# Kernel optimization log

Hardware: AMD Instinct MI355X
Metric: run time of the kernel (lower is better)

## Reference

```python
import jax, jax.numpy as jnp
import numpy as np

B, N, D, H, DH = 1, 192, 128, 4, 32
INNER = H * DH  # == D


def _ln(x, g, b):
    mu = x.mean(-1, keepdims=True)
    var = ((x - mu) ** 2).mean(-1, keepdims=True)
    return (x - mu) * jax.lax.rsqrt(var + 1e-5) * g + b


def _axial(x, row, lng, lnb, wq, wkv, wo, bo, wg, bg, wb):
    # x: (B, N, N, D). row=True: attend along axis 2 (rows as batch);
    # row=False: attend along axis 1 (columns as batch).
    scale = DH ** -0.5
    # edge bias from RAW x (edges are not layer-normed in the torch code)
    bias = jnp.einsum('bijd,dh->bhij', x, wb)            # (B, H, N, N)
    xn = _ln(x, lng, lnb)
    xa = xn if row else jnp.swapaxes(xn, 1, 2)           # (B, R, S, D)
    q = (xa @ wq).reshape(B, N, N, H, DH) * scale
    kv = (xa @ wkv).reshape(B, N, N, 2, H, DH)           # chunk(2): k then v
    k, v = kv[..., 0, :, :], kv[..., 1, :, :]
    # scores: (B, R, H, q, k); same bias matrix broadcast over every row/col R
    dots = jnp.einsum('brqhe,brkhe->brhqk', q, k) + bias[:, None]
    attn = jax.nn.softmax(dots, axis=-1)
    o = jnp.einsum('brhqk,brkhe->brqhe', attn, v).reshape(B, N, N, INNER)
    gates = jax.nn.sigmoid(xa @ wg + bg)                 # sigmoid gating on pre-attn x
    out = (o * gates) @ wo + bo
    return out if row else jnp.swapaxes(out, 1, 2)


def setup_inputs() -> dict:
    key = jax.random.key(0)
    ks = iter(jax.random.split(key, 32))

    def w(shape, s=0.02):
        return jax.random.normal(next(ks), shape, dtype=jnp.float32) * s

    inp = {"x": jax.random.normal(next(ks), (B, N, N, D), dtype=jnp.float32)}
    for sfx in ("o", "i"):  # outgoing (row) / ingoing (col) triangle attention
        inp[f"lng_{sfx}"] = jnp.ones((D,), jnp.float32)
        inp[f"lnb_{sfx}"] = jnp.zeros((D,), jnp.float32)
        inp[f"wq_{sfx}"] = w((D, INNER))
        inp[f"wkv_{sfx}"] = w((D, 2 * INNER))
        inp[f"wo_{sfx}"] = w((INNER, D))
        inp[f"bo_{sfx}"] = jnp.zeros((D,), jnp.float32)
        inp[f"wg_{sfx}"] = w((D, INNER))
        inp[f"bg_{sfx}"] = jnp.ones((INNER,), jnp.float32)  # gating bias init = 1
        inp[f"wb_{sfx}"] = w((D, H))
    inp["lng_f"] = jnp.ones((D,), jnp.float32)
    inp["lnb_f"] = jnp.zeros((D,), jnp.float32)
    inp["w1"] = w((D, 8 * D))      # dim -> dim*mult*2, mult=4
    inp["b1"] = jnp.zeros((8 * D,), jnp.float32)
    inp["w2"] = w((4 * D, D))
    inp["b2"] = jnp.zeros((D,), jnp.float32)
    return inp


def reference(x, lng_o, lnb_o, wq_o, wkv_o, wo_o, bo_o, wg_o, bg_o, wb_o,
              lng_i, lnb_i, wq_i, wkv_i, wo_i, bo_i, wg_i, bg_i, wb_i,
              lng_f, lnb_f, w1, b1, w2, b2):
    x = _axial(x, True, lng_o, lnb_o, wq_o, wkv_o, wo_o, bo_o, wg_o, bg_o, wb_o) + x
    x = _axial(x, False, lng_i, lnb_i, wq_i, wkv_i, wo_i, bo_i, wg_i, bg_i, wb_i) + x
    xn = _ln(x, lng_f, lnb_f)
    h = xn @ w1 + b1
    a, g = jnp.split(h, 2, axis=-1)   # GEGLU: x * gelu(gates), exact gelu
    ff = (a * jax.nn.gelu(g, approximate=False)) @ w2 + b2
    return x + ff
```

## Files before the change

kernel.cpp:

```cpp
#include <hip/hip_runtime.h>
#include <hip/hip_bf16.h>
#include <math.h>

constexpr int NSEQ = 192;
constexpr int DIM  = 128;
constexpr int NH   = 4;
constexpr int DHEAD = 32;
constexpr int MROWS = NSEQ * NSEQ;

typedef __hip_bfloat16 bf16;
typedef __attribute__((ext_vector_type(8))) short bf16x8;
typedef __attribute__((ext_vector_type(4))) float f32x4;
typedef unsigned int u32;

__device__ __forceinline__ void gload16(const void* g, void* l) {
    __builtin_amdgcn_global_load_lds(
        (const __attribute__((address_space(1))) u32*)g,
        (__attribute__((address_space(3))) u32*)l, 16, 0, 0);
}

__device__ __forceinline__ short f2bs(float f) {
    __hip_bfloat16 h = __float2bfloat16(f);
    return *(short*)&h;
}

__global__ __launch_bounds__(256)
void convert_weights(const float* __restrict__ wq_o, const float* __restrict__ wkv_o,
                     const float* __restrict__ wg_o,
                     const float* __restrict__ wq_i, const float* __restrict__ wkv_i,
                     const float* __restrict__ wg_i,
                     const float* __restrict__ wo_o, const float* __restrict__ wo_i,
                     const float* __restrict__ w1, const float* __restrict__ b1,
                     const float* __restrict__ w2,
                     bf16* __restrict__ WQKVG_O, bf16* __restrict__ WQKVG_I,
                     bf16* __restrict__ WOT_O, bf16* __restrict__ WOT_I,
                     bf16* __restrict__ W1PT, bf16* __restrict__ W2T,
                     float* __restrict__ B1P)
{
    int idx = blockIdx.x * 256 + threadIdx.x;
    const float scale = 0.17677669529663689f;
    if (idx < 131072) {
        int s = idx >> 16, i = idx & 65535;
        int r = i >> 7, d = i & 127;
        const float* wq  = s ? wq_i  : wq_o;
        const float* wkv = s ? wkv_i : wkv_o;
        const float* wg  = s ? wg_i  : wg_o;
        float v;
        if (r < 128)      v = wq[d * 128 + r] * scale;
        else if (r < 384) v = wkv[d * 256 + (r - 128)];
        else              v = wg[d * 128 + (r - 384)];
        (s ? WQKVG_I : WQKVG_O)[i] = __float2bfloat16(v);
    } else if (idx < 163840) {
        int i = idx - 131072; int s = i >> 14; i &= 16383;
        int r = i >> 7, d = i & 127;
        (s ? WOT_I : WOT_O)[i] = __float2bfloat16((s ? wo_i : wo_o)[d * 128 + r]);
    } else if (idx < 294912) {
        int i = idx - 163840;
        int r = i >> 7, d = i & 127;
        int col = (r & 1) ? 512 + (r >> 1) : (r >> 1);
        W1PT[i] = __float2bfloat16(w1[d * 1024 + col]);
    } else if (idx < 360448) {
        int i = idx - 294912;
        int n = i >> 9, k = i & 511;
        W2T[i] = __float2bfloat16(w2[k * 128 + n]);
    } else if (idx < 361472) {
        int r = idx - 360448;
        B1P[r] = b1[(r & 1) ? 512 + (r >> 1) : (r >> 1)];
    }
}

__global__ __launch_bounds__(256)
void ln_bias_kernel(const float* __restrict__ x, const float* __restrict__ g,
                    const float* __restrict__ b, const float* __restrict__ wb,
                    bf16* __restrict__ xa, float* __restrict__ bias)
{
    int wid  = threadIdx.x >> 6;
    int lane = threadIdx.x & 63;
    int row  = blockIdx.x * 4 + wid;
    const float* xr = x + (size_t)row * DIM;
    float x0 = xr[lane], x1 = xr[lane + 64];
    float s = x0 + x1, sq = x0 * x0 + x1 * x1;
    #pragma unroll
    for (int off = 32; off > 0; off >>= 1) {
        s  += __shfl_down(s, off);
        sq += __shfl_down(sq, off);
    }
    s = __shfl(s, 0); sq = __shfl(sq, 0);
    float mu  = s * (1.0f / 128.0f);
    float var = sq * (1.0f / 128.0f) - mu * mu;
    float rs  = rsqrtf(var + 1e-5f);
    float y0 = (x0 - mu) * rs * g[lane]      + b[lane];
    float y1 = (x1 - mu) * rs * g[lane + 64] + b[lane + 64];
    bf16* yr = xa + (size_t)row * DIM;
    yr[lane]      = __float2bfloat16(y0);
    yr[lane + 64] = __float2bfloat16(y1);
    #pragma unroll
    for (int h = 0; h < NH; ++h) {
        float bh = x0 * wb[lane * NH + h] + x1 * wb[(lane + 64) * NH + h];
        #pragma unroll
        for (int off = 32; off > 0; off >>= 1) bh += __shfl_down(bh, off);
        if (lane == 0) bias[(size_t)h * MROWS + row] = bh;
    }
}

enum { EPI_QKVG = 0, EPI_OUT = 1, EPI_GEGLU = 2, EPI_FF2 = 3 };

template<int EPI, int BM, int K>
__global__ __launch_bounds__(256, 4)
void mfma_gemm(const bf16* __restrict__ A, const bf16* __restrict__ BT,
               const float* __restrict__ e_bias,
               const float* __restrict__ e_resid,
               float* __restrict__ e_outf,
               bf16* __restrict__ e_outb,
               bf16* __restrict__ e_outb2,
               const float* __restrict__ lng,
               const float* __restrict__ lnb,
               const float* __restrict__ wbp,
               float* __restrict__ biasb,
               bf16* __restrict__ xa,
               int trans)
{
    constexpr int MREP  = BM / 32;
    constexpr int AB    = BM * 128;
    constexpr int STAGE = AB + 16384;
    constexpr int EPIB  = (BM / 2) * 512;
    constexpr int LDSB  = STAGE > EPIB ? STAGE : EPIB;
    __shared__ char sm[LDSB];
    char* asb = sm;
    char* bsb = sm + AB;
    float* eb = (float*)sm;

    int tid = threadIdx.x;
    int l = tid & 63, w = tid >> 6;
    int wr = w >> 1, wc = w & 1;
    int m0 = blockIdx.x * BM, n0 = blockIdx.y * 128;
    int fr = l & 15, g = l >> 4;
    int lr8 = l >> 3;
    int satom = (l & 7) ^ lr8;

    f32x4 acc[MREP][4] = {};

    for (int k0 = 0; k0 < K; k0 += 64) {
        #pragma unroll
        for (int i = 0; i < BM / 32; ++i)
            gload16(A + (size_t)(m0 + i * 32 + w * 8 + lr8) * K + k0 + satom * 8,
                    asb + i * 4096 + w * 1024);
        #pragma unroll
        for (int i = 0; i < 4; ++i)
            gload16(BT + (size_t)(n0 + i * 32 + w * 8 + lr8) * K + k0 + satom * 8,
                    bsb + i * 4096 + w * 1024);
        __syncthreads();
        #pragma unroll
        for (int kk = 0; kk < 2; ++kk) {
            bf16x8 af[MREP], bfr[4];
            #pragma unroll
            for (int mi = 0; mi < MREP; ++mi) {
                int r = wr * (BM / 2) + mi * 16 + fr;
                af[mi] = *(const bf16x8*)(asb + r * 128 + ((kk * 64 + g * 16) ^ ((r & 7) << 4)));
            }
            #pragma unroll
            for (int ni = 0; ni < 4; ++ni) {
                int r = wc * 64 + ni * 16 + fr;
                bfr[ni] = *(const bf16x8*)(bsb + r * 128 + ((kk * 64 + g * 16) ^ ((r & 7) << 4)));
            }
            #pragma unroll
            for (int mi = 0; mi < MREP; ++mi)
                #pragma unroll
                for (int ni = 0; ni < 4; ++ni)
                    acc[mi][ni] = __builtin_amdgcn_mfma_f32_16x16x32_bf16(
                        af[mi], bfr[ni], acc[mi][ni], 0, 0, 0);
        }
        __syncthreads();
    }

    #pragma unroll
    for (int rr = 0; rr < 2; ++rr) {
        if (wr == rr) {
            #pragma unroll
            for (int mi = 0; mi < MREP; ++mi)
                #pragma unroll
                for (int ni = 0; ni < 4; ++ni)
                    #pragma unroll
                    for (int j = 0; j < 4; ++j) {
                        int rl = mi * 16 + g * 4 + j;
                        int cl = wc * 64 + ni * 16 + fr;
                        int a  = cl >> 2;
                        int pa = (((a >> 2) + (a & 3)) & 7) | ((a & 3) << 3);
                        eb[rl * 128 + pa * 4 + (cl & 3)] = acc[mi][ni][j];
                    }
        }
        __syncthreads();
        #pragma unroll
        for (int p = 0; p < BM / 64; ++p) {
            int c = tid + p * 256;
            int row_l = c >> 3, ch = c & 7;
            int grow = m0 + rr * (BM / 2) + row_l;
            int gc0 = ch * 16;
            float v[16];
            #pragma unroll
            for (int q = 0; q < 4; ++q) {
                int pa = ((ch + q) & 7) + q * 8;
                f32x4 t4 = *(const f32x4*)&eb[row_l * 128 + pa * 4];
                v[q * 4 + 0] = t4[0]; v[q * 4 + 1] = t4[1];
                v[q * 4 + 2] = t4[2]; v[q * 4 + 3] = t4[3];
            }
            if (EPI == EPI_QKVG) {
                int seg = blockIdx.y;
                short o16[16];
                if (seg < 3) {
                    #pragma unroll
                    for (int i = 0; i < 16; ++i) o16[i] = f2bs(v[i]);
                    int h = ch >> 1, e0 = (ch & 1) * 16;
                    bf16* dst = e_outb + ((size_t)(seg * NH + h) * MROWS + grow) * DHEAD + e0;
                    *(uint4*)dst = *(uint4*)o16;
                    *(uint4*)(dst + 8) = *(uint4*)(o16 + 8);
                } else {
                    #pragma unroll
                    for (int i = 0; i < 16; ++i)
                        o16[i] = f2bs(1.0f / (1.0f + __expf(-(v[i] + e_bias[gc0 + i]))));
                    bf16* dst = e_outb2 + (size_t)grow * DIM + gc0;
                    *(uint4*)dst = *(uint4*)o16;
                    *(uint4*)(dst + 8) = *(uint4*)(o16 + 8);
                }
            } else if (EPI == EPI_OUT) {
                int orow  = trans ? ((grow % NSEQ) * NSEQ + grow / NSEQ) : grow;
                int xarow = (grow % NSEQ) * NSEQ + grow / NSEQ;
                const float* rp = e_resid + (size_t)orow * DIM + gc0;
                float* op = e_outf + (size_t)orow * DIM + gc0;
                #pragma unroll
                for (int q = 0; q < 4; ++q) {
                    float4 r4 = *(const float4*)(rp + q * 4);
                    v[q*4+0] += e_bias[gc0 + q*4 + 0] + r4.x;
                    v[q*4+1] += e_bias[gc0 + q*4 + 1] + r4.y;
                    v[q*4+2] += e_bias[gc0 + q*4 + 2] + r4.z;
                    v[q*4+3] += e_bias[gc0 + q*4 + 3] + r4.w;
                    *(float4*)(op + q * 4) = make_float4(v[q*4+0], v[q*4+1], v[q*4+2], v[q*4+3]);
                }
                float s1 = 0.f, s2 = 0.f;
                #pragma unroll
                for (int i = 0; i < 16; ++i) { s1 += v[i]; s2 += v[i] * v[i]; }
                #pragma unroll
                for (int off = 1; off < 8; off <<= 1) {
                    s1 += __shfl_xor(s1, off);
                    s2 += __shfl_xor(s2, off);
                }
                float mu  = s1 * (1.0f / 128.0f);
                float var = s2 * (1.0f / 128.0f) - mu * mu;
                float rs  = rsqrtf(var + 1e-5f);
                short o16[16];
                #pragma unroll
                for (int i = 0; i < 16; ++i)
                    o16[i] = f2bs((v[i] - mu) * rs * lng[gc0 + i] + lnb[gc0 + i]);
                bf16* xd = xa + (size_t)xarow * DIM + gc0;
                *(uint4*)xd = *(uint4*)o16;
                *(uint4*)(xd + 8) = *(uint4*)(o16 + 8);
                if (wbp) {
                    float bh[NH] = {};
                    #pragma unroll
                    for (int i = 0; i < 16; ++i) {
                        float vv = v[i];
                        #pragma unroll
                        for (int h = 0; h < NH; ++h)
                            bh[h] = fmaf(vv, wbp[(gc0 + i) * NH + h], bh[h]);
                    }
                    #pragma unroll
                    for (int off = 1; off < 8; off <<= 1)
                        #pragma unroll
                        for (int h = 0; h < NH; ++h) bh[h] += __shfl_xor(bh[h], off);
                    if (ch == 0)
                        #pragma unroll
                        for (int h = 0; h < NH; ++h)
                            biasb[(size_t)h * MROWS + grow] = bh[h];
                }
            } else if (EPI == EPI_FF2) {
                const float* rp = e_resid + (size_t)grow * DIM + gc0;
                float* op = e_outf + (size_t)grow * DIM + gc0;
                #pragma unroll
                for (int q = 0; q < 4; ++q) {
                    float4 r4 = *(const float4*)(rp + q * 4);
                    float4 o4;
                    o4.x = v[q*4+0] + e_bias[gc0 + q*4 + 0] + r4.x;
                    o4.y = v[q*4+1] + e_bias[gc0 + q*4 + 1] + r4.y;
                    o4.z = v[q*4+2] + e_bias[gc0 + q*4 + 2] + r4.z;
                    o4.w = v[q*4+3] + e_bias[gc0 + q*4 + 3] + r4.w;
                    *(float4*)(op + q * 4) = o4;
                }
            } else {
                short o8[8];
                #pragma unroll
                for (int t = 0; t < 8; ++t) {
                    float a  = v[2*t]     + e_bias[n0 + gc0 + 2*t];
                    float gg = v[2*t + 1] + e_bias[n0 + gc0 + 2*t + 1];
                    float y  = 1.5957691216f * (gg + 0.044715f * gg * gg * gg);
                    float ge = gg / (1.0f + __expf(-y));
                    o8[t] = f2bs(a * ge);
                }
                *(uint4*)(e_outb + (size_t)grow * 512 + ((n0 + gc0) >> 1)) = *(uint4*)o8;
            }
        }
        __syncthreads();
    }
}

__global__ __launch_bounds__(256)
void attn_mfma_kernel(const bf16* __restrict__ Qh, const bf16* __restrict__ Kh,
                      const bf16* __restrict__ Vh, const float* __restrict__ BIAS,
                      const bf16* __restrict__ G, bf16* __restrict__ TMP)
{
    __shared__ unsigned short vtp[32][200];
    int h = blockIdx.x / NSEQ;
    int r = blockIdx.x % NSEQ;
    int t = threadIdx.x;
    int l = t & 63;
    int w = t >> 6;

    const bf16* vbase = Vh + ((size_t)h * MROWS + (size_t)r * NSEQ) * DHEAD;
    #pragma unroll
    for (int i = 0; i < 6; ++i) {
        int q4 = t + i * 256;
        int k = q4 >> 3, e0 = (q4 & 7) * 4;
        uint2 v = *(const uint2*)(vbase + (size_t)k * DHEAD + e0);
        int kk = k & 31, sup = k >> 5;
        int col = sup * 32 + ((kk & 15) >> 2) * 8 + (kk & 3) + ((kk >> 4) << 2);
        const unsigned short* vs = (const unsigned short*)&v;
        #pragma unroll
        for (int j = 0; j < 4; ++j) vtp[e0 + j][col] = vs[j];
    }
    __syncthreads();

    int fr = l & 15, g = l >> 4;
    int q0 = w * 48;
    const bf16*  qbase = Qh + ((size_t)h * MROWS + (size_t)r * NSEQ) * DHEAD;
    const bf16*  kbase = Kh + ((size_t)h * MROWS + (size_t)r * NSEQ) * DHEAD;
    const float* bbase = BIAS + (size_t)h * MROWS;

    bf16x8 qf[3];
    #pragma unroll
    for (int i = 0; i < 3; ++i)
        qf[i] = *(const bf16x8*)(qbase + (size_t)(q0 + i * 16 + fr) * DHEAD + g * 8);

    f32x4 ot[3][2] = {};
    float m_[3] = {-1e30f, -1e30f, -1e30f};
    float s_[3] = {};

    for (int sup = 0; sup < 6; ++sup) {
        bf16x8 kf0 = *(const bf16x8*)(kbase + (size_t)(sup * 32 + fr) * DHEAD + g * 8);
        bf16x8 kf1 = *(const bf16x8*)(kbase + (size_t)(sup * 32 + 16 + fr) * DHEAD + g * 8);
        bf16x8 pb[3];
        #pragma unroll
        for (int qt = 0; qt < 3; ++qt) {
            f32x4 z = {};
            f32x4 s0 = __builtin_amdgcn_mfma_f32_16x16x32_bf16(kf0, qf[qt], z, 0, 0, 0);
            f32x4 s1 = __builtin_amdgcn_mfma_f32_16x16x32_bf16(kf1, qf[qt], z, 0, 0, 0);
            const float* bp = bbase + (size_t)(q0 + qt * 16 + fr) * NSEQ + sup * 32 + g * 4;
            float4 b0 = *(const float4*)bp;
            float4 b1 = *(const float4*)(bp + 16);
            s0[0] += b0.x; s0[1] += b0.y; s0[2] += b0.z; s0[3] += b0.w;
            s1[0] += b1.x; s1[1] += b1.y; s1[2] += b1.z; s1[3] += b1.w;
            float tmax = fmaxf(fmaxf(fmaxf(s0[0], s0[1]), fmaxf(s0[2], s0[3])),
                               fmaxf(fmaxf(s1[0], s1[1]), fmaxf(s1[2], s1[3])));
            tmax = fmaxf(tmax, __shfl_xor(tmax, 16));
            tmax = fmaxf(tmax, __shfl_xor(tmax, 32));
            if (__any(tmax > m_[qt] + 8.0f)) {
                float mn = fmaxf(m_[qt], tmax);
                float c = __expf(m_[qt] - mn);
                s_[qt] *= c; ot[qt][0] *= c; ot[qt][1] *= c;
                m_[qt] = mn;
            }
            float p[8];
            #pragma unroll
            for (int j = 0; j < 4; ++j) p[j]     = __expf(s0[j] - m_[qt]);
            #pragma unroll
            for (int j = 0; j < 4; ++j) p[4 + j] = __expf(s1[j] - m_[qt]);
            s_[qt] += ((p[0] + p[1]) + (p[2] + p[3])) + ((p[4] + p[5]) + (p[6] + p[7]));
            bf16x8 pk;
            #pragma unroll
            for (int j = 0; j < 8; ++j) pk[j] = f2bs(p[j]);
            pb[qt] = pk;
        }
        #pragma unroll
        for (int et = 0; et < 2; ++et) {
            bf16x8 vf = *(const bf16x8*)(&vtp[et * 16 + fr][sup * 32 + g * 8]);
            #pragma unroll
            for (int qt = 0; qt < 3; ++qt)
                ot[qt][et] = __builtin_amdgcn_mfma_f32_16x16x32_bf16(vf, pb[qt], ot[qt][et], 0, 0, 0);
        }
    }

    #pragma unroll
    for (int qt = 0; qt < 3; ++qt) {
        float sq = s_[qt];
        sq += __shfl_xor(sq, 16);
        sq += __shfl_xor(sq, 32);
        float inv = 1.0f / sq;
        int q = q0 + qt * 16 + fr;
        size_t row = (size_t)r * NSEQ + q;
        #pragma unroll
        for (int et = 0; et < 2; ++et) {
            int e0 = h * DHEAD + et * 16 + g * 4;
            const bf16* gp = G + row * DIM + e0;
            u32 g01 = *(const u32*)gp;
            u32 g23 = *(const u32*)(gp + 2);
            float gx0 = __uint_as_float((g01 & 0xffffu) << 16);
            float gx1 = __uint_as_float(g01 & 0xffff0000u);
            float gx2 = __uint_as_float((g23 & 0xffffu) << 16);
            float gx3 = __uint_as_float(g23 & 0xffff0000u);
            short o4[4];
            o4[0] = f2bs(ot[qt][et][0] * inv * gx0);
            o4[1] = f2bs(ot[qt][et][1] * inv * gx1);
            o4[2] = f2bs(ot[qt][et][2] * inv * gx2);
            o4[3] = f2bs(ot[qt][et][3] * inv * gx3);
            *(uint2*)(TMP + row * DIM + e0) = *(uint2*)o4;
        }
    }
}

extern "C" void kernel_launch(void* const* d_in, const int* in_sizes, int n_in,
                              void* d_out, int out_size, void* d_ws, size_t ws_size,
                              hipStream_t stream) {
    const float* x     = (const float*)d_in[0];
    const float* lng_o = (const float*)d_in[1];
    const float* lnb_o = (const float*)d_in[2];
    const float* wq_o  = (const float*)d_in[3];
    const float* wkv_o = (const float*)d_in[4];
    const float* wo_o  = (const float*)d_in[5];
    const float* bo_o  = (const float*)d_in[6];
    const float* wg_o  = (const float*)d_in[7];
    const float* bg_o  = (const float*)d_in[8];
    const float* wb_o  = (const float*)d_in[9];
    const float* lng_i = (const float*)d_in[10];
    const float* lnb_i = (const float*)d_in[11];
    const float* wq_i  = (const float*)d_in[12];
    const float* wkv_i = (const float*)d_in[13];
    const float* wo_i  = (const float*)d_in[14];
    const float* bo_i  = (const float*)d_in[15];
    const float* wg_i  = (const float*)d_in[16];
    const float* bg_i  = (const float*)d_in[17];
    const float* wb_i  = (const float*)d_in[18];
    const float* lng_f = (const float*)d_in[19];
    const float* lnb_f = (const float*)d_in[20];
    const float* w1    = (const float*)d_in[21];
    const float* b1    = (const float*)d_in[22];
    const float* w2    = (const float*)d_in[23];
    const float* b2    = (const float*)d_in[24];

    const size_t T = (size_t)MROWS * DIM;
    char* base = (char*)d_ws;
    bf16*  XA    = (bf16*)base;  base += T * 2;
    float* X     = (float*)base; base += T * 4;
    bf16*  QKVb  = (bf16*)base;  base += 3 * T * 2;
    bf16*  Gb    = (bf16*)base;  base += T * 2;
    float* BIASb = (float*)base; base += (size_t)NH * MROWS * 4;
    bf16*  TMP   = (bf16*)base;  base += T * 2;
    bf16*  WQKVG_O = (bf16*)base; base += 512 * 128 * 2;
    bf16*  WQKVG_I = (bf16*)base; base += 512 * 128 * 2;
    bf16*  WOT_O   = (bf16*)base; base += 128 * 128 * 2;
    bf16*  WOT_I   = (bf16*)base; base += 128 * 128 * 2;
    bf16*  W1PT    = (bf16*)base; base += 1024 * 128 * 2;
    bf16*  W2T     = (bf16*)base; base += 128 * 512 * 2;
    float* B1P     = (float*)base; base += 1024 * 4;
    bf16*  H2      = (bf16*)QKVb;
    bf16*  Qhp = QKVb;
    bf16*  Khp = QKVb + T;
    bf16*  Vhp = QKVb + 2 * T;

    convert_weights<<<1412, 256, 0, stream>>>(wq_o, wkv_o, wg_o, wq_i, wkv_i, wg_i,
                                              wo_o, wo_i, w1, b1, w2,
                                              WQKVG_O, WQKVG_I, WOT_O, WOT_I,
                                              W1PT, W2T, B1P);

    dim3 gQKVG(MROWS / 128, 4), gOUT(MROWS / 128, 1), gW1(MROWS / 128, 8);
    dim3 gFF2(MROWS / 64, 1);

    ln_bias_kernel<<<MROWS / 4, 256, 0, stream>>>(x, lng_o, lnb_o, wb_o, XA, BIASb);
    mfma_gemm<EPI_QKVG, 128, 128><<<gQKVG, 256, 0, stream>>>(
        XA, WQKVG_O, bg_o, nullptr, nullptr, QKVb, Gb,
        nullptr, nullptr, nullptr, nullptr, nullptr, 0);
    attn_mfma_kernel<<<NSEQ * NH, 256, 0, stream>>>(Qhp, Khp, Vhp, BIASb, Gb, TMP);
    mfma_gemm<EPI_OUT, 128, 128><<<gOUT, 256, 0, stream>>>(
        TMP, WOT_O, bo_o, x, X, nullptr, nullptr,
        lng_i, lnb_i, wb_i, BIASb, XA, 0);

    mfma_gemm<EPI_QKVG, 128, 128><<<gQKVG, 256, 0, stream>>>(
        XA, WQKVG_I, bg_i, nullptr, nullptr, QKVb, Gb,
        nullptr, nullptr, nullptr, nullptr, nullptr, 0);
    attn_mfma_kernel<<<NSEQ * NH, 256, 0, stream>>>(Qhp, Khp, Vhp, BIASb, Gb, TMP);
    mfma_gemm<EPI_OUT, 128, 128><<<gOUT, 256, 0, stream>>>(
        TMP, WOT_I, bo_i, X, X, nullptr, nullptr,
        lng_f, lnb_f, nullptr, nullptr, XA, 1);

    mfma_gemm<EPI_GEGLU, 128, 128><<<gW1, 256, 0, stream>>>(
        XA, W1PT, B1P, nullptr, nullptr, H2, nullptr,
        nullptr, nullptr, nullptr, nullptr, nullptr, 0);
    mfma_gemm<EPI_FF2, 64, 512><<<gFF2, 256, 0, stream>>>(
        H2, W2T, b2, X, (float*)d_out, nullptr, nullptr,
        nullptr, nullptr, nullptr, nullptr, nullptr, 0);
}
```

Before: 231.2 us.

## Store residual stream in bf16, merge prep kernels, shrink output-GEMM tiles

Keeps the running residual X and a bf16 copy of the input as bf16 instead of fp32, halving residual read/write traffic in the output and FF2 epilogues. Merges the weight conversion and first layernorm/bias kernels into one launch, vectorizes the layernorm loads and stores, and lowers the output-projection GEMM tile from 128 to 64 rows so more blocks launch. The cost is lower residual precision, since bf16 rounding accumulates across the layers, plus a different block-size tradeoff for the output GEMM.

Result: faster. 193.0 us (-16.5%).

```diff
diff --git a/kernel.cpp b/kernel.cpp
--- a/kernel.cpp
+++ b/kernel.cpp
@@ -23,63 +23,66 @@
     __hip_bfloat16 h = __float2bfloat16(f);
     return *(short*)&h;
 }
+__device__ __forceinline__ float bs2f(unsigned short s) {
+    return __uint_as_float(((u32)s) << 16);
+}
 
 __global__ __launch_bounds__(256)
-void convert_weights(const float* __restrict__ wq_o, const float* __restrict__ wkv_o,
-                     const float* __restrict__ wg_o,
-                     const float* __restrict__ wq_i, const float* __restrict__ wkv_i,
-                     const float* __restrict__ wg_i,
-                     const float* __restrict__ wo_o, const float* __restrict__ wo_i,
-                     const float* __restrict__ w1, const float* __restrict__ b1,
-                     const float* __restrict__ w2,
-                     bf16* __restrict__ WQKVG_O, bf16* __restrict__ WQKVG_I,
-                     bf16* __restrict__ WOT_O, bf16* __restrict__ WOT_I,
-                     bf16* __restrict__ W1PT, bf16* __restrict__ W2T,
-                     float* __restrict__ B1P)
+void prep_kernel(const float* __restrict__ wq_o, const float* __restrict__ wkv_o,
+                 const float* __restrict__ wg_o,
+                 const float* __restrict__ wq_i, const float* __restrict__ wkv_i,
+                 const float* __restrict__ wg_i,
+                 const float* __restrict__ wo_o, const float* __restrict__ wo_i,
+                 const float* __restrict__ w1, const float* __restrict__ b1,
+                 const float* __restrict__ w2,
+                 bf16* __restrict__ WQKVG_O, bf16* __restrict__ WQKVG_I,
+                 bf16* __restrict__ WOT_O, bf16* __restrict__ WOT_I,
+                 bf16* __restrict__ W1PT, bf16* __restrict__ W2T,
+                 float* __restrict__ B1P,
+                 const float* __restrict__ x, const float* __restrict__ lng,
+                 const float* __restrict__ lnb, const float* __restrict__ wb,
+                 bf16* __restrict__ xa, float* __restrict__ bias,
+                 bf16* __restrict__ xb)
 {
-    int idx = blockIdx.x * 256 + threadIdx.x;
-    const float scale = 0.17677669529663689f;
-    if (idx < 131072) {
-        int s = idx >> 16, i = idx & 65535;
-        int r = i >> 7, d = i & 127;
-        const float* wq  = s ? wq_i  : wq_o;
-        const float* wkv = s ? wkv_i : wkv_o;
-        const float* wg  = s ? wg_i  : wg_o;
-        float v;
-        if (r < 128)      v = wq[d * 128 + r] * scale;
-        else if (r < 384) v = wkv[d * 256 + (r - 128)];
-        else              v = wg[d * 128 + (r - 384)];
-        (s ? WQKVG_I : WQKVG_O)[i] = __float2bfloat16(v);
-    } else if (idx < 163840) {
-        int i = idx - 131072; int s = i >> 14; i &= 16383;
-        int r = i >> 7, d = i & 127;
-        (s ? WOT_I : WOT_O)[i] = __float2bfloat16((s ? wo_i : wo_o)[d * 128 + r]);
-    } else if (idx < 294912) {
-        int i = idx - 163840;
-        int r = i >> 7, d = i & 127;
-        int col = (r & 1) ? 512 + (r >> 1) : (r >> 1);
-        W1PT[i] = __float2bfloat16(w1[d * 1024 + col]);
-    } else if (idx < 360448) {
-        int i = idx - 294912;
-        int n = i >> 9, k = i & 511;
-        W2T[i] = __float2bfloat16(w2[k * 128 + n]);
-    } else if (idx < 361472) {
-        int r = idx - 360448;
-        B1P[r] = b1[(r & 1) ? 512 + (r >> 1) : (r >> 1)];
-    }
-}
-
-__global__ __launch_bounds__(256)
-void ln_bias_kernel(const float* __restrict__ x, const float* __restrict__ g,
-                    const float* __restrict__ b, const float* __restrict__ wb,
-                    bf16* __restrict__ xa, float* __restrict__ bias)
-{
+    if (blockIdx.x < 1412) {
+        int idx = blockIdx.x * 256 + threadIdx.x;
+        const float scale = 0.17677669529663689f;
+        if (idx < 131072) {
+            int s = idx >> 16, i = idx & 65535;
+            int r = i >> 7, d = i & 127;
+            const float* wq  = s ? wq_i  : wq_o;
+            const float* wkv = s ? wkv_i : wkv_o;
+            const float* wg  = s ? wg_i  : wg_o;
+            float v;
+            if (r < 128)      v = wq[d * 128 + r] * scale;
+            else if (r < 384) v = wkv[d * 256 + (r - 128)];
+            else              v = wg[d * 128 + (r - 384)];
+            (s ? WQKVG_I : WQKVG_O)[i] = __float2bfloat16(v);
+        } else if (idx < 163840) {
+            int i = idx - 131072; int s = i >> 14; i &= 16383;
+            int r = i >> 7, d = i & 127;
+            (s ? WOT_I : WOT_O)[i] = __float2bfloat16((s ? wo_i : wo_o)[d * 128 + r]);
+        } else if (idx < 294912) {
+            int i = idx - 163840;
+            int r = i >> 7, d = i & 127;
+            int col = (r & 1) ? 512 + (r >> 1) : (r >> 1);
+            W1PT[i] = __float2bfloat16(w1[d * 1024 + col]);
+        } else if (idx < 360448) {
+            int i = idx - 294912;
+            int n = i >> 9, k = i & 511;
+            W2T[i] = __float2bfloat16(w2[k * 128 + n]);
+        } else if (idx < 361472) {
+            int r = idx - 360448;
+            B1P[r] = b1[(r & 1) ? 512 + (r >> 1) : (r >> 1)];
+        }
+        return;
+    }
     int wid  = threadIdx.x >> 6;
     int lane = threadIdx.x & 63;
-    int row  = blockIdx.x * 4 + wid;
+    int row  = (blockIdx.x - 1412) * 4 + wid;
     const float* xr = x + (size_t)row * DIM;
-    float x0 = xr[lane], x1 = xr[lane + 64];
-    float s = x0 + x1, sq = x0 * x0 + x1 * x1;
+    float2 xv = *(const float2*)(xr + lane * 2);
+    float s = xv.x + xv.y, sq = xv.x * xv.x + xv.y * xv.y;
     #pragma unroll
     for (int off = 32; off > 0; off >>= 1) {
         s  += __shfl_down(s, off);
@@ -89,14 +92,19 @@
     float mu  = s * (1.0f / 128.0f);
     float var = sq * (1.0f / 128.0f) - mu * mu;
     float rs  = rsqrtf(var + 1e-5f);
-    float y0 = (x0 - mu) * rs * g[lane]      + b[lane];
-    float y1 = (x1 - mu) * rs * g[lane + 64] + b[lane + 64];
-    bf16* yr = xa + (size_t)row * DIM;
-    yr[lane]      = __float2bfloat16(y0);
-    yr[lane + 64] = __float2bfloat16(y1);
+    float2 gv = *(const float2*)(lng + lane * 2);
+    float2 bv = *(const float2*)(lnb + lane * 2);
+    float y0 = (xv.x - mu) * rs * gv.x + bv.x;
+    float y1 = (xv.y - mu) * rs * gv.y + bv.y;
+    u32 packed = (u32)(unsigned short)f2bs(y0) | ((u32)(unsigned short)f2bs(y1) << 16);
+    *(u32*)(xa + (size_t)row * DIM + lane * 2) = packed;
+    u32 packedx = (u32)(unsigned short)f2bs(xv.x) | ((u32)(unsigned short)f2bs(xv.y) << 16);
+    *(u32*)(xb + (size_t)row * DIM + lane * 2) = packedx;
+    float4 w0 = *(const float4*)(wb + lane * 8);
+    float4 w1v = *(const float4*)(wb + lane * 8 + 4);
     #pragma unroll
     for (int h = 0; h < NH; ++h) {
-        float bh = x0 * wb[lane * NH + h] + x1 * wb[(lane + 64) * NH + h];
+        float bh = xv.x * ((const float*)&w0)[h] + xv.y * ((const float*)&w1v)[h];
         #pragma unroll
         for (int off = 32; off > 0; off >>= 1) bh += __shfl_down(bh, off);
         if (lane == 0) bias[(size_t)h * MROWS + row] = bh;
@@ -109,7 +117,7 @@
 __global__ __launch_bounds__(256, 4)
 void mfma_gemm(const bf16* __restrict__ A, const bf16* __restrict__ BT,
                const float* __restrict__ e_bias,
-               const float* __restrict__ e_resid,
+               const bf16* __restrict__ e_residb,
                float* __restrict__ e_outf,
                bf16* __restrict__ e_outb,
                bf16* __restrict__ e_outb2,
@@ -225,17 +233,19 @@
             } else if (EPI == EPI_OUT) {
                 int orow  = trans ? ((grow % NSEQ) * NSEQ + grow / NSEQ) : grow;
                 int xarow = (grow % NSEQ) * NSEQ + grow / NSEQ;
-                const float* rp = e_resid + (size_t)orow * DIM + gc0;
-                float* op = e_outf + (size_t)orow * DIM + gc0;
-                #pragma unroll
-                for (int q = 0; q < 4; ++q) {
-                    float4 r4 = *(const float4*)(rp + q * 4);
-                    v[q*4+0] += e_bias[gc0 + q*4 + 0] + r4.x;
-                    v[q*4+1] += e_bias[gc0 + q*4 + 1] + r4.y;
-                    v[q*4+2] += e_bias[gc0 + q*4 + 2] + r4.z;
-                    v[q*4+3] += e_bias[gc0 + q*4 + 3] + r4.w;
-                    *(float4*)(op + q * 4) = make_float4(v[q*4+0], v[q*4+1], v[q*4+2], v[q*4+3]);
+                unsigned short r16[16];
+                const bf16* rp = e_residb + (size_t)orow * DIM + gc0;
+                *(uint4*)r16 = *(const uint4*)rp;
+                *(uint4*)(r16 + 8) = *(const uint4*)(rp + 8);
+                short o16[16];
+                #pragma unroll
+                for (int i = 0; i < 16; ++i) {
+                    v[i] += e_bias[gc0 + i] + bs2f(r16[i]);
+                    o16[i] = f2bs(v[i]);
                 }
+                bf16* xo = e_outb + (size_t)orow * DIM + gc0;
+                *(uint4*)xo = *(uint4*)o16;
+                *(uint4*)(xo + 8) = *(uint4*)(o16 + 8);
                 float s1 = 0.f, s2 = 0.f;
                 #pragma unroll
                 for (int i = 0; i < 16; ++i) { s1 += v[i]; s2 += v[i] * v[i]; }
@@ -247,7 +257,6 @@
                 float mu  = s1 * (1.0f / 128.0f);
                 float var = s2 * (1.0f / 128.0f) - mu * mu;
                 float rs  = rsqrtf(var + 1e-5f);
-                short o16[16];
                 #pragma unroll
                 for (int i = 0; i < 16; ++i)
                     o16[i] = f2bs((v[i] - mu) * rs * lng[gc0 + i] + lnb[gc0 + i]);
@@ -273,16 +282,18 @@
                             biasb[(size_t)h * MROWS + grow] = bh[h];
                 }
             } else if (EPI == EPI_FF2) {
-                const float* rp = e_resid + (size_t)grow * DIM + gc0;
+                unsigned short r16[16];
+                const bf16* rp = e_residb + (size_t)grow * DIM + gc0;
+                *(uint4*)r16 = *(const uint4*)rp;
+                *(uint4*)(r16 + 8) = *(const uint4*)(rp + 8);
                 float* op = e_outf + (size_t)grow * DIM + gc0;
                 #pragma unroll
                 for (int q = 0; q < 4; ++q) {
-                    float4 r4 = *(const float4*)(rp + q * 4);
                     float4 o4;
-                    o4.x = v[q*4+0] + e_bias[gc0 + q*4 + 0] + r4.x;
-                    o4.y = v[q*4+1] + e_bias[gc0 + q*4 + 1] + r4.y;
-                    o4.z = v[q*4+2] + e_bias[gc0 + q*4 + 2] + r4.z;
-                    o4.w = v[q*4+3] + e_bias[gc0 + q*4 + 3] + r4.w;
+                    o4.x = v[q*4+0] + e_bias[gc0 + q*4 + 0] + bs2f(r16[q*4+0]);
+                    o4.y = v[q*4+1] + e_bias[gc0 + q*4 + 1] + bs2f(r16[q*4+1]);
+                    o4.z = v[q*4+2] + e_bias[gc0 + q*4 + 2] + bs2f(r16[q*4+2]);
+                    o4.w = v[q*4+3] + e_bias[gc0 + q*4 + 3] + bs2f(r16[q*4+3]);
                     *(float4*)(op + q * 4) = o4;
                 }
             } else {
@@ -447,7 +458,8 @@
     const size_t T = (size_t)MROWS * DIM;
     char* base = (char*)d_ws;
     bf16*  XA    = (bf16*)base;  base += T * 2;
-    float* X     = (float*)base; base += T * 4;
+    bf16*  XB    = (bf16*)base;  base += T * 2;
+    bf16*  X     = (bf16*)base;  base += T * 2;
     bf16*  QKVb  = (bf16*)base;  base += 3 * T * 2;
     bf16*  Gb    = (bf16*)base;  base += T * 2;
     float* BIASb = (float*)base; base += (size_t)NH * MROWS * 4;
@@ -464,29 +476,28 @@
     bf16*  Khp = QKVb + T;
     bf16*  Vhp = QKVb + 2 * T;
 
-    convert_weights<<<1412, 256, 0, stream>>>(wq_o, wkv_o, wg_o, wq_i, wkv_i, wg_i,
-                                              wo_o, wo_i, w1, b1, w2,
-                                              WQKVG_O, WQKVG_I, WOT_O, WOT_I,
-                                              W1PT, W2T, B1P);
-
-    dim3 gQKVG(MROWS / 128, 4), gOUT(MROWS / 128, 1), gW1(MROWS / 128, 8);
+    prep_kernel<<<1412 + MROWS / 4, 256, 0, stream>>>(
+        wq_o, wkv_o, wg_o, wq_i, wkv_i, wg_i, wo_o, wo_i, w1, b1, w2,
+        WQKVG_O, WQKVG_I, WOT_O, WOT_I, W1PT, W2T, B1P,
+        x, lng_o, lnb_o, wb_o, XA, BIASb, XB);
+
+    dim3 gQKVG(MROWS / 128, 4), gOUT(MROWS / 64, 1), gW1(MROWS / 128, 8);
     dim3 gFF2(MROWS / 64, 1);
 
-    ln_bias_kernel<<<MROWS / 4, 256, 0, stream>>>(x, lng_o, lnb_o, wb_o, XA, BIASb);
     mfma_gemm<EPI_QKVG, 128, 128><<<gQKVG, 256, 0, stream>>>(
         XA, WQKVG_O, bg_o, nullptr, nullptr, QKVb, Gb,
         nullptr, nullptr, nullptr, nullptr, nullptr, 0);
     attn_mfma_kernel<<<NSEQ * NH, 256, 0, stream>>>(Qhp, Khp, Vhp, BIASb, Gb, TMP);
-    mfma_gemm<EPI_OUT, 128, 128><<<gOUT, 256, 0, stream>>>(
-        TMP, WOT_O, bo_o, x, X, nullptr, nullptr,
+    mfma_gemm<EPI_OUT, 64, 128><<<gOUT, 256, 0, stream>>>(
+        TMP, WOT_O, bo_o, XB, nullptr, X, nullptr,
         lng_i, lnb_i, wb_i, BIASb, XA, 0);
 
     mfma_gemm<EPI_QKVG, 128, 128><<<gQKVG, 256, 0, stream>>>(
         XA, WQKVG_I, bg_i, nullptr, nullptr, QKVb, Gb,
         nullptr, nullptr, nullptr, nullptr, nullptr, 0);
     attn_mfma_kernel<<<NSEQ * NH, 256, 0, stream>>>(Qhp, Khp, Vhp, BIASb, Gb, TMP);
-    mfma_gemm<EPI_OUT, 128, 128><<<gOUT, 256, 0, stream>>>(
-        TMP, WOT_I, bo_i, X, X, nullptr, nullptr,
+    mfma_gemm<EPI_OUT, 64, 128><<<gOUT, 256, 0, stream>>>(
+        TMP, WOT_I, bo_i, X, nullptr, X, nullptr,
         lng_f, lnb_f, nullptr, nullptr, XA, 1);
 
     mfma_gemm<EPI_GEGLU, 128, 128><<<gW1, 256, 0, stream>>>(
```
